# Kernel optimization log

Hardware: AMD Instinct MI355X
Metric: run time of the kernel (lower is better)

Reference implementation:

```python
import jax, jax.numpy as jnp
import numpy as np

H = 12            # num_heads
GRID = 14         # sqrt(num_patches)
NP_ = GRID * GRID # num_patches = 196


def _relative_position_index():
    coords = np.stack(np.meshgrid(np.arange(GRID), np.arange(GRID), indexing='ij'))  # [2,14,14]
    flat = coords.reshape(2, -1)                                   # [2,196]
    rel = flat[:, :, None] - flat[:, None, :]                      # [2,196,196]
    rel = rel.transpose(1, 2, 0).astype(np.int32)                  # [196,196,2]
    rel[..., 0] += GRID - 1
    rel[..., 1] += GRID - 1
    rel[..., 0] *= 2 * GRID - 1
    return rel.sum(-1)                                             # [196,196] in [0,729)


def setup_inputs() -> dict:
    key = jax.random.key(0)
    k1, k2, k3, k4 = jax.random.split(key, 4)
    B, N, C = 64, NP_ + 1, 768
    return {
        'x': jax.random.normal(k1, (B, N, C), dtype=jnp.float32),
        'w_qkv': jax.random.normal(k2, (3 * C, C), dtype=jnp.float32) * 0.02,
        'w_proj': jax.random.normal(k3, (C, C), dtype=jnp.float32) * 0.02,
        'b_proj': jnp.zeros((C,), dtype=jnp.float32),
        # torch inits the table to zeros; use small randn so the bias path is exercised
        'rpb_table': jax.random.normal(k4, ((2 * GRID - 1) ** 2, H), dtype=jnp.float32) * 0.02,
        'rel_idx': jnp.asarray(_relative_position_index()),
    }


def reference(x, w_qkv, w_proj, b_proj, rpb_table, rel_idx):
    B, N, C = x.shape
    hd = C // H
    scale = hd ** -0.5
    qkv = (x @ w_qkv.T).reshape(B, N, 3, H, hd).transpose(2, 0, 3, 1, 4)  # [3,B,H,N,hd]
    q, k, v = qkv[0] * scale, qkv[1], qkv[2]
    attn = jnp.einsum('bhqd,bhkd->bhqk', q, k)                            # [B,H,N,N]
    bias = rpb_table[rel_idx.reshape(-1)].reshape(NP_, NP_, H).transpose(2, 0, 1)  # [H,196,196]
    attn = attn.at[:, :, 1:, 1:].add(bias[None])                          # skip CLS row/col
    attn = jax.nn.softmax(attn, axis=-1)
    out = jnp.einsum('bhqk,bhkd->bqhd', attn, v).reshape(B, N, C)
    return out @ w_proj.T + b_proj
```

## Files before the change

### kernel.cpp

```cpp
#include <hip/hip_runtime.h>

typedef float f32x4 __attribute__((ext_vector_type(4)));
typedef short short8 __attribute__((ext_vector_type(8)));

#define DEVI static __device__ __forceinline__

DEVI ushort f2bf(float f) {
  unsigned u = __builtin_bit_cast(unsigned, f);
  u += 0x7fffu + ((u >> 16) & 1u);
  return (ushort)(u >> 16);
}

DEVI short8 pack8(float4 a, float4 b) {
  union { ushort u[8]; short8 v; } t;
  t.u[0] = f2bf(a.x); t.u[1] = f2bf(a.y); t.u[2] = f2bf(a.z); t.u[3] = f2bf(a.w);
  t.u[4] = f2bf(b.x); t.u[5] = f2bf(b.y); t.u[6] = f2bf(b.z); t.u[7] = f2bf(b.w);
  return t.v;
}

DEVI f32x4 MFMA16(short8 a, short8 b, f32x4 c) {
  return __builtin_amdgcn_mfma_f32_16x16x32_bf16(a, b, c, 0, 0, 0);
}

DEVI void gld16(const ushort* g, ushort* l) {
  __builtin_amdgcn_global_load_lds(
      (const __attribute__((address_space(1))) unsigned int*)g,
      (__attribute__((address_space(3))) unsigned int*)l, 16, 0, 0);
}

__global__ void prep_all(const float* __restrict__ table, const int* __restrict__ rel_idx,
                         float* __restrict__ bias,
                         const float* __restrict__ x, ushort* __restrict__ xbf,
                         const float* __restrict__ wq, ushort* __restrict__ wqb,
                         const float* __restrict__ wp, ushort* __restrict__ wpb) {
  const int bid = blockIdx.x, tid = threadIdx.x;
  if (bid < 2028) {
    int i = bid * 256 + tid;
    int k = i % 208;
    int t = i / 208;
    int q = t % 208;
    int h = t / 208;
    float v;
    if (k >= 197) v = -1e30f;
    else if (q == 0 || k == 0 || q >= 197) v = 0.0f;
    else v = table[rel_idx[(q - 1) * 196 + (k - 1)] * 12 + h];
    bias[i] = v;
  } else if (bid < 6756) {
    int i = (bid - 2028) * 256 + tid;
    float4 a = ((const float4*)x)[i * 2];
    float4 b = ((const float4*)x)[i * 2 + 1];
    ((short8*)xbf)[i] = pack8(a, b);
  } else if (bid < 7620) {
    int i = (bid - 6756) * 256 + tid;
    float4 a = ((const float4*)wq)[i * 2];
    float4 b = ((const float4*)wq)[i * 2 + 1];
    ((short8*)wqb)[i] = pack8(a, b);
  } else {
    int i = (bid - 7620) * 256 + tid;
    float4 a = ((const float4*)wp)[i * 2];
    float4 b = ((const float4*)wp)[i * 2 + 1];
    ((short8*)wpb)[i] = pack8(a, b);
  }
}

#define BARRIER() { asm volatile("" ::: "memory"); __builtin_amdgcn_s_barrier(); asm volatile("" ::: "memory"); }
#define VMC(N) asm volatile("s_waitcnt vmcnt(" #N ")" ::: "memory")
#define NOP

template <int MODE, int NBN>
__launch_bounds__(512, 2)
__global__ void gemm8p(const ushort* __restrict__ A, const ushort* __restrict__ B,
                       ushort* __restrict__ q, ushort* __restrict__ k,
                       ushort* __restrict__ v,
                       const float* __restrict__ bprj, float* __restrict__ out) {
  __shared__ __align__(16) ushort AS[32768];
  __shared__ __align__(16) ushort BS[32768];

  const int tid = threadIdx.x;
  const int lane = tid & 63, wid = tid >> 6;
  const int wm = wid >> 2, wn = wid & 3;
  const int l15 = lane & 15, l4 = lane >> 4;

  const int nwg = gridDim.x;
  const int qc = nwg >> 3, rc = nwg & 7;
  const int xcd = blockIdx.x & 7, sub = blockIdx.x >> 3;
  const int wgid = (xcd < rc ? xcd * (qc + 1) : rc * (qc + 1) + (xcd - rc) * qc) + sub;
  const int bn = wgid % NBN, bm = wgid / NBN;

  const int lr = lane >> 3;
  const int cg = lane & 7;
  const ushort* pa[2][2];
  const ushort* pb[2][2];
#pragma unroll
  for (int h = 0; h < 2; h++) {
#pragma unroll
    for (int j = 0; j < 2; j++) {
      int rhl = wid * 8 + lr + j * 64;
      int scol = (cg ^ (rhl & 7)) * 8;
      long garow = (long)bm * 256 + (rhl >> 4) * 32 + h * 16 + (rhl & 15);
      if (garow > 12607) garow = 12607;
      pa[h][j] = A + garow * 768 + scol;
      pb[h][j] = B + ((long)bn * 256 + h * 128 + rhl) * 768 + scol;
    }
  }

  const int cs0 = (l4 * 8) ^ ((l15 & 7) << 3);

  f32x4 acc[8][4];
#pragma unroll
  for (int m = 0; m < 8; m++)
#pragma unroll
    for (int n = 0; n < 4; n++) acc[m][n] = (f32x4)0.0f;

#define SA(BUF, H, KT) { gld16(pa[H][0] + (KT) * 64, AS + (BUF) * 16384 + (H) * 8192 + wid * 512);        \
                         gld16(pa[H][1] + (KT) * 64, AS + (BUF) * 16384 + (H) * 8192 + wid * 512 + 4096); }
#define SB(BUF, H, KT) { gld16(pb[H][0] + (KT) * 64, BS + (BUF) * 16384 + (H) * 8192 + wid * 512);        \
                         gld16(pb[H][1] + (KT) * 64, BS + (BUF) * 16384 + (H) * 8192 + wid * 512 + 4096); }

#define PHASE(BUF, FH, KK, STG, WAITC)                                                        \
  {                                                                                           \
    short8 af[4], bv[4];                                                                      \
    const int cko = cs0 ^ ((KK) << 5);                                                        \
    _Pragma("unroll") for (int j = 0; j < 4; j++)                                             \
      af[j] = *(const short8*)&AS[(BUF) * 16384 + (FH) * 8192 + (wm * 4 + j) * 1024 +         \
                                  l15 * 64 + cko];                                            \
    _Pragma("unroll") for (int n = 0; n < 4; n++)                                             \
      bv[n] = *(const short8*)&BS[(BUF) * 16384 + (wn >> 1) * 8192 +                          \
                                  ((wn & 1) * 64 + n * 16 + l15) * 64 + cko];                 \
    STG;                                                                                      \
    WAITC;                                                                                    \
    BARRIER();                                                                                \
    __builtin_amdgcn_s_setprio(1);                                                            \
    _Pragma("unroll") for (int j = 0; j < 4; j++)                                             \
      _Pragma("unroll") for (int n = 0; n < 4; n++)                                           \
        acc[(FH) + 2 * j][n] = MFMA16(af[j], bv[n], acc[(FH) + 2 * j][n]);                    \
    __builtin_amdgcn_s_setprio(0);                                                            \
    BARRIER();                                                                                \
  }

  SA(0, 0, 0) SA(0, 1, 0) SB(0, 0, 0) SB(0, 1, 0) SA(1, 0, 1)
  VMC(2);
  BARRIER();

  for (int i = 0; i < 5; ++i) {
    const int t1 = 2 * i + 1, t2 = 2 * i + 2, t3 = 2 * i + 3;
    PHASE(0, 0, 0, SA(1, 1, t1), NOP)
    PHASE(0, 1, 0, SB(1, 0, t1), NOP)
    PHASE(0, 0, 1, SB(1, 1, t1), NOP)
    PHASE(0, 1, 1, SA(0, 0, t2), VMC(2))
    PHASE(1, 0, 0, SA(0, 1, t2), NOP)
    PHASE(1, 1, 0, SB(0, 0, t2), NOP)
    PHASE(1, 0, 1, SB(0, 1, t2), NOP)
    PHASE(1, 1, 1, SA(1, 0, t3), VMC(2))
  }
  PHASE(0, 0, 0, SA(1, 1, 11), NOP)
  PHASE(0, 1, 0, SB(1, 0, 11), NOP)
  PHASE(0, 0, 1, SB(1, 1, 11), NOP)
  PHASE(0, 1, 1, NOP, VMC(0))
  PHASE(1, 0, 0, NOP, NOP)
  PHASE(1, 1, 0, NOP, NOP)
  PHASE(1, 0, 1, NOP, NOP)
  PHASE(1, 1, 1, NOP, NOP)

  if (MODE == 0) {
    const int c6 = (bn * 256 + wn * 64) >> 6;
    const int s = c6 / 12, hh = c6 % 12;
    ushort* dst = (s == 0) ? q : ((s == 1) ? k : v);
    const float qs = (s == 0) ? 0.125f : 1.0f;
#pragma unroll
    for (int f = 0; f < 8; f++) {
#pragma unroll
      for (int r = 0; r < 4; r++) {
        int gm = bm * 256 + wm * 128 + f * 16 + l4 * 4 + r;
        if (gm >= 12608) continue;
        int b = gm / 197;
        int ns = gm - b * 197;
        size_t base = (size_t)((b * 12 + hh) * 197 + ns) * 64;
#pragma unroll
        for (int n = 0; n < 4; n++)
          dst[base + n * 16 + l15] = f2bf(acc[f][n][r] * qs);
      }
    }
  } else {
    float bb[4];
#pragma unroll
    for (int n = 0; n < 4; n++) bb[n] = bprj[bn * 256 + wn * 64 + n * 16 + l15];
#pragma unroll
    for (int f = 0; f < 8; f++) {
#pragma unroll
      for (int r = 0; r < 4; r++) {
        int gm = bm * 256 + wm * 128 + f * 16 + l4 * 4 + r;
        if (gm >= 12608) continue;
#pragma unroll
        for (int n = 0; n < 4; n++)
          out[(size_t)gm * 768 + bn * 256 + wn * 64 + n * 16 + l15] = acc[f][n][r] + bb[n];
      }
    }
  }
#undef SA
#undef SB
#undef PHASE
}

__launch_bounds__(512)
__global__ void attn(const ushort* __restrict__ qws, const ushort* __restrict__ kws,
                     const ushort* __restrict__ vws, const float* __restrict__ biasws,
                     ushort* __restrict__ aout) {
  __shared__ __align__(16) ushort Ks[208 * 72];
  __shared__ __align__(16) ushort Vt[64 * 232];
  __shared__ __align__(16) ushort Ps[8 * 16 * 232];

  const int bh = blockIdx.x;
  const int b = bh / 12;
  const int h = bh - b * 12;
  const ushort* qb = qws + (size_t)bh * 197 * 64;
  const ushort* kb = kws + (size_t)bh * 197 * 64;
  const ushort* vb = vws + (size_t)bh * 197 * 64;

  const int tid = threadIdx.x;
  const int lane = tid & 63, wid = tid >> 6;
  const int l15 = lane & 15, l4 = lane >> 4;

  for (int c = tid; c < 208 * 8; c += 512) {
    int n = c >> 3, col = (c & 7) << 3;
    short8 v = (short8)0;
    if (n < 197) v = *(const short8*)(kb + n * 64 + col);
    *(short8*)&Ks[n * 72 + col] = v;
  }
  for (int c = tid; c < 224 * 8; c += 512) {
    int n = c % 224;
    int d0 = (c / 224) << 3;
    ushort tmp[8] = {0, 0, 0, 0, 0, 0, 0, 0};
    if (n < 197) {
      short8 v = *(const short8*)(vb + n * 64 + d0);
#pragma unroll
      for (int j = 0; j < 8; j++) tmp[j] = (ushort)v[j];
    }
#pragma unroll
    for (int j = 0; j < 8; j++) Vt[(d0 + j) * 232 + n] = tmp[j];
  }
  __syncthreads();

  ushort* pb = &Ps[wid * (16 * 232)];
  const float* biasb = biasws + (size_t)h * 208 * 208;

  for (int t = wid; t < 13; t += 8) {
    const int q0 = t * 16;
    int qr = q0 + l15; if (qr > 196) qr = 196;
    short8 aq0 = *(const short8*)(qb + qr * 64 + (l4 << 3));
    short8 aq1 = *(const short8*)(qb + qr * 64 + 32 + (l4 << 3));

    f32x4 sc[13];
    __builtin_amdgcn_s_setprio(1);
#pragma unroll
    for (int ct = 0; ct < 13; ct++) {
      short8 b0 = *(const short8*)&Ks[(ct * 16 + l15) * 72 + (l4 << 3)];
      short8 b1 = *(const short8*)&Ks[(ct * 16 + l15) * 72 + 32 + (l4 << 3)];
      f32x4 s = (f32x4)0.0f;
      s = MFMA16(aq0, b0, s);
      s = MFMA16(aq1, b1, s);
      sc[ct] = s;
    }
    __builtin_amdgcn_s_setprio(0);

    float mx[4] = {-1e38f, -1e38f, -1e38f, -1e38f};
#pragma unroll
    for (int ct = 0; ct < 13; ct++) {
#pragma unroll
      for (int r = 0; r < 4; r++) {
        float bv = biasb[(q0 + l4 * 4 + r) * 208 + ct * 16 + l15];
        float v = sc[ct][r] + bv;
        sc[ct][r] = v;
        mx[r] = fmaxf(mx[r], v);
      }
    }
#pragma unroll
    for (int r = 0; r < 4; r++) {
      mx[r] = fmaxf(mx[r], __shfl_xor(mx[r], 1));
      mx[r] = fmaxf(mx[r], __shfl_xor(mx[r], 2));
      mx[r] = fmaxf(mx[r], __shfl_xor(mx[r], 4));
      mx[r] = fmaxf(mx[r], __shfl_xor(mx[r], 8));
    }
    float sum[4] = {0.f, 0.f, 0.f, 0.f};
#pragma unroll
    for (int ct = 0; ct < 13; ct++) {
#pragma unroll
      for (int r = 0; r < 4; r++) {
        float p = __expf(sc[ct][r] - mx[r]);
        sc[ct][r] = p;
        sum[r] += p;
      }
    }
#pragma unroll
    for (int r = 0; r < 4; r++) {
      sum[r] += __shfl_xor(sum[r], 1);
      sum[r] += __shfl_xor(sum[r], 2);
      sum[r] += __shfl_xor(sum[r], 4);
      sum[r] += __shfl_xor(sum[r], 8);
    }

#pragma unroll
    for (int ct = 0; ct < 13; ct++)
#pragma unroll
      for (int r = 0; r < 4; r++)
        pb[(l4 * 4 + r) * 232 + ct * 16 + l15] = f2bf(sc[ct][r]);
#pragma unroll
    for (int r = 0; r < 4; r++)
      pb[(l4 * 4 + r) * 232 + 208 + l15] = 0;

    short8 pa[7];
#pragma unroll
    for (int kk = 0; kk < 7; kk++)
      pa[kk] = *(const short8*)&pb[l15 * 232 + kk * 32 + (l4 << 3)];
    f32x4 o[4];
    __builtin_amdgcn_s_setprio(1);
#pragma unroll
    for (int dt = 0; dt < 4; dt++) {
      f32x4 acc = (f32x4)0.0f;
#pragma unroll
      for (int kk = 0; kk < 7; kk++) {
        short8 bv = *(const short8*)&Vt[(dt * 16 + l15) * 232 + kk * 32 + (l4 << 3)];
        acc = MFMA16(pa[kk], bv, acc);
      }
      o[dt] = acc;
    }
    __builtin_amdgcn_s_setprio(0);

    float rs[4];
#pragma unroll
    for (int r = 0; r < 4; r++) rs[r] = 1.0f / sum[r];
#pragma unroll
    for (int dt = 0; dt < 4; dt++) {
#pragma unroll
      for (int r = 0; r < 4; r++) {
        int row = q0 + l4 * 4 + r;
        if (row < 197) {
          float v = o[dt][r] * rs[r];
          aout[(size_t)(b * 197 + row) * 768 + h * 64 + dt * 16 + l15] = f2bf(v);
        }
      }
    }
  }
}

extern "C" void kernel_launch(void* const* d_in, const int* in_sizes, int n_in,
                              void* d_out, int out_size, void* d_ws, size_t ws_size,
                              hipStream_t stream) {
  const float* x      = (const float*)d_in[0];
  const float* w_qkv  = (const float*)d_in[1];
  const float* w_proj = (const float*)d_in[2];
  const float* b_proj = (const float*)d_in[3];
  const float* rpb    = (const float*)d_in[4];
  const int*   relidx = (const int*)d_in[5];
  float* out = (float*)d_out;

  char* ws = (char*)d_ws;
  const size_t HB = (size_t)12608 * 768 * 2;
  ushort* xbf   = (ushort*)(ws);
  ushort* qws   = (ushort*)(ws + HB);
  ushort* kws   = (ushort*)(ws + 2 * HB);
  ushort* vws   = (ushort*)(ws + 3 * HB);
  float*  bias  = (float*)(ws + 4 * HB);
  ushort* wqkvb = (ushort*)(ws + 4 * HB + 2076672);
  ushort* wprjb = (ushort*)(ws + 4 * HB + 2076672 + 3538944);
  ushort* aout  = xbf;

  hipLaunchKernelGGL(prep_all, dim3(7908), dim3(256), 0, stream,
                     rpb, relidx, bias, x, xbf, w_qkv, wqkvb, w_proj, wprjb);
  hipLaunchKernelGGL((gemm8p<0, 9>), dim3(9 * 50), dim3(512), 0, stream,
                     xbf, wqkvb, qws, kws, vws, nullptr, nullptr);
  hipLaunchKernelGGL(attn, dim3(768), dim3(512), 0, stream, qws, kws, vws, bias, aout);
  hipLaunchKernelGGL((gemm8p<1, 3>), dim3(3 * 50), dim3(512), 0, stream,
                     aout, wprjb, nullptr, nullptr, nullptr, b_proj, out);
}
```

Before: 147.7 us.

## Restructure GEMM LDS tiling into quadrant phases and store bias as bf16

Reworks the GEMM main loop so each phase computes a 64x32 quadrant over the full 64-wide k-slice. Staging loads are regrouped per quadrant with a new swizzle, and vmcnt waits are tuned so loads overlap with MFMAs more finely. Separately, the relative-position bias buffer is stored as bf16 instead of fp32, halving its reads in the attention kernel. The bf16 bias loses some precision, and the -1e30 mask value is rounded to bf16.

Result: no change. 149.6 us (+1.3%).

```diff
diff --git a/kernel.cpp b/kernel.cpp
--- a/kernel.cpp
+++ b/kernel.cpp
@@ -9,6 +9,11 @@
   unsigned u = __builtin_bit_cast(unsigned, f);
   u += 0x7fffu + ((u >> 16) & 1u);
   return (ushort)(u >> 16);
+}
+
+DEVI float b2f(ushort u) {
+  unsigned x = ((unsigned)u) << 16;
+  return __builtin_bit_cast(float, x);
 }
 
 DEVI short8 pack8(float4 a, float4 b) {
@@ -28,8 +33,11 @@
       (__attribute__((address_space(3))) unsigned int*)l, 16, 0, 0);
 }
 
+#define VMC(N) asm volatile("s_waitcnt vmcnt(" #N ")" ::: "memory")
+#define LGK0() asm volatile("s_waitcnt lgkmcnt(0)" ::: "memory")
+
 __global__ void prep_all(const float* __restrict__ table, const int* __restrict__ rel_idx,
-                         float* __restrict__ bias,
+                         ushort* __restrict__ bias,
                          const float* __restrict__ x, ushort* __restrict__ xbf,
                          const float* __restrict__ wq, ushort* __restrict__ wqb,
                          const float* __restrict__ wp, ushort* __restrict__ wpb) {
@@ -44,7 +52,7 @@
     if (k >= 197) v = -1e30f;
     else if (q == 0 || k == 0 || q >= 197) v = 0.0f;
     else v = table[rel_idx[(q - 1) * 196 + (k - 1)] * 12 + h];
-    bias[i] = v;
+    bias[i] = f2bf(v);
   } else if (bid < 6756) {
     int i = (bid - 2028) * 256 + tid;
     float4 a = ((const float4*)x)[i * 2];
@@ -63,16 +71,12 @@
   }
 }
 
-#define BARRIER() { asm volatile("" ::: "memory"); __builtin_amdgcn_s_barrier(); asm volatile("" ::: "memory"); }
-#define VMC(N) asm volatile("s_waitcnt vmcnt(" #N ")" ::: "memory")
-#define NOP
-
 template <int MODE, int NBN>
 __launch_bounds__(512, 2)
-__global__ void gemm8p(const ushort* __restrict__ A, const ushort* __restrict__ B,
-                       ushort* __restrict__ q, ushort* __restrict__ k,
-                       ushort* __restrict__ v,
-                       const float* __restrict__ bprj, float* __restrict__ out) {
+__global__ void gemm8(const ushort* __restrict__ A, const ushort* __restrict__ B,
+                      ushort* __restrict__ q, ushort* __restrict__ k,
+                      ushort* __restrict__ v,
+                      const float* __restrict__ bprj, float* __restrict__ out) {
   __shared__ __align__(16) ushort AS[32768];
   __shared__ __align__(16) ushort BS[32768];
 
@@ -87,24 +91,28 @@
   const int wgid = (xcd < rc ? xcd * (qc + 1) : rc * (qc + 1) + (xcd - rc) * qc) + sub;
   const int bn = wgid % NBN, bm = wgid / NBN;
 
-  const int lr = lane >> 3;
-  const int cg = lane & 7;
+  const int sr = lane >> 3;
+  const int scol = ((lane & 7) ^ sr) << 3;
   const ushort* pa[2][2];
-  const ushort* pb[2][2];
+  const ushort* pbv[2][2];
+  int la[2][2], lb[2][2];
 #pragma unroll
   for (int h = 0; h < 2; h++) {
 #pragma unroll
     for (int j = 0; j < 2; j++) {
-      int rhl = wid * 8 + lr + j * 64;
-      int scol = (cg ^ (rhl & 7)) * 8;
-      long garow = (long)bm * 256 + (rhl >> 4) * 32 + h * 16 + (rhl & 15);
-      if (garow > 12607) garow = 12607;
-      pa[h][j] = A + garow * 768 + scol;
-      pb[h][j] = B + ((long)bn * 256 + h * 128 + rhl) * 768 + scol;
-    }
-  }
-
-  const int cs0 = (l4 * 8) ^ ((l15 & 7) << 3);
+      int rowA = j * 128 + h * 64 + wid * 8 + sr;
+      long ga = (long)bm * 256 + rowA;
+      if (ga > 12607) ga = 12607;
+      pa[h][j] = A + ga * 768 + scol;
+      la[h][j] = h * 4096 + wid * 512 + j * 8192;
+      int rowB = j * 128 + (wid >> 2) * 64 + h * 32 + (wid & 3) * 8 + sr;
+      pbv[h][j] = B + ((long)bn * 256 + rowB) * 768 + scol;
+      lb[h][j] = (wid >> 2) * 4096 + h * 2048 + (wid & 3) * 512 + j * 8192;
+    }
+  }
+
+  const int c0 = ((l4 ^ (l15 & 7)) << 3);
+  const int c1 = (((4 | l4) ^ (l15 & 7)) << 3);
 
   f32x4 acc[8][4];
 #pragma unroll
@@ -112,55 +120,66 @@
 #pragma unroll
     for (int n = 0; n < 4; n++) acc[m][n] = (f32x4)0.0f;
 
-#define SA(BUF, H, KT) { gld16(pa[H][0] + (KT) * 64, AS + (BUF) * 16384 + (H) * 8192 + wid * 512);        \
-                         gld16(pa[H][1] + (KT) * 64, AS + (BUF) * 16384 + (H) * 8192 + wid * 512 + 4096); }
-#define SB(BUF, H, KT) { gld16(pb[H][0] + (KT) * 64, BS + (BUF) * 16384 + (H) * 8192 + wid * 512);        \
-                         gld16(pb[H][1] + (KT) * 64, BS + (BUF) * 16384 + (H) * 8192 + wid * 512 + 4096); }
-
-#define PHASE(BUF, FH, KK, STG, WAITC)                                                        \
-  {                                                                                           \
-    short8 af[4], bv[4];                                                                      \
-    const int cko = cs0 ^ ((KK) << 5);                                                        \
-    _Pragma("unroll") for (int j = 0; j < 4; j++)                                             \
-      af[j] = *(const short8*)&AS[(BUF) * 16384 + (FH) * 8192 + (wm * 4 + j) * 1024 +         \
-                                  l15 * 64 + cko];                                            \
-    _Pragma("unroll") for (int n = 0; n < 4; n++)                                             \
-      bv[n] = *(const short8*)&BS[(BUF) * 16384 + (wn >> 1) * 8192 +                          \
-                                  ((wn & 1) * 64 + n * 16 + l15) * 64 + cko];                 \
-    STG;                                                                                      \
-    WAITC;                                                                                    \
-    BARRIER();                                                                                \
-    __builtin_amdgcn_s_setprio(1);                                                            \
-    _Pragma("unroll") for (int j = 0; j < 4; j++)                                             \
-      _Pragma("unroll") for (int n = 0; n < 4; n++)                                           \
-        acc[(FH) + 2 * j][n] = MFMA16(af[j], bv[n], acc[(FH) + 2 * j][n]);                    \
-    __builtin_amdgcn_s_setprio(0);                                                            \
-    BARRIER();                                                                                \
-  }
-
-  SA(0, 0, 0) SA(0, 1, 0) SB(0, 0, 0) SB(0, 1, 0) SA(1, 0, 1)
-  VMC(2);
-  BARRIER();
+#define STA(BUF, H, KO) { gld16(pa[H][0] + (KO), AS + (BUF) * 16384 + la[H][0]); \
+                          gld16(pa[H][1] + (KO), AS + (BUF) * 16384 + la[H][1]); }
+#define STB(BUF, H, KO) { gld16(pbv[H][0] + (KO), BS + (BUF) * 16384 + lb[H][0]); \
+                          gld16(pbv[H][1] + (KO), BS + (BUF) * 16384 + lb[H][1]); }
+
+#define PHASE(BUF, MQ, NQ, STG, WAITC)                                          \
+  {                                                                             \
+    __builtin_amdgcn_sched_barrier(0);                                          \
+    short8 af0[4], af1[4], bq0[2], bq1[2];                                      \
+    const int abo = (BUF) * 16384 + (wm * 128 + (MQ) * 64 + l15) * 64;          \
+    const int bbo = (BUF) * 16384 + (wn * 64 + (NQ) * 32 + l15) * 64;           \
+    _Pragma("unroll") for (int j = 0; j < 4; j++)                               \
+      af0[j] = *(const short8*)&AS[abo + j * 1024 + c0];                        \
+    _Pragma("unroll") for (int j = 0; j < 4; j++)                               \
+      af1[j] = *(const short8*)&AS[abo + j * 1024 + c1];                        \
+    _Pragma("unroll") for (int n = 0; n < 2; n++)                               \
+      bq0[n] = *(const short8*)&BS[bbo + n * 1024 + c0];                        \
+    _Pragma("unroll") for (int n = 0; n < 2; n++)                               \
+      bq1[n] = *(const short8*)&BS[bbo + n * 1024 + c1];                        \
+    STG                                                                         \
+    WAITC;                                                                      \
+    __builtin_amdgcn_s_barrier();                                               \
+    LGK0();                                                                     \
+    __builtin_amdgcn_sched_barrier(0);                                          \
+    __builtin_amdgcn_s_setprio(1);                                              \
+    _Pragma("unroll") for (int j = 0; j < 4; j++)                               \
+      _Pragma("unroll") for (int n = 0; n < 2; n++) {                           \
+        acc[(MQ) * 4 + j][(NQ) * 2 + n] =                                       \
+            MFMA16(af0[j], bq0[n], acc[(MQ) * 4 + j][(NQ) * 2 + n]);            \
+        acc[(MQ) * 4 + j][(NQ) * 2 + n] =                                       \
+            MFMA16(af1[j], bq1[n], acc[(MQ) * 4 + j][(NQ) * 2 + n]);            \
+      }                                                                         \
+    __builtin_amdgcn_s_setprio(0);                                              \
+    __builtin_amdgcn_s_barrier();                                               \
+  }
+
+  STA(0, 0, 0) STB(0, 0, 0) STA(0, 1, 0) STB(0, 1, 0)
+  STA(1, 0, 64) STB(1, 0, 64)
+  VMC(8);
+  __builtin_amdgcn_s_barrier();
 
   for (int i = 0; i < 5; ++i) {
-    const int t1 = 2 * i + 1, t2 = 2 * i + 2, t3 = 2 * i + 3;
-    PHASE(0, 0, 0, SA(1, 1, t1), NOP)
-    PHASE(0, 1, 0, SB(1, 0, t1), NOP)
-    PHASE(0, 0, 1, SB(1, 1, t1), NOP)
-    PHASE(0, 1, 1, SA(0, 0, t2), VMC(2))
-    PHASE(1, 0, 0, SA(0, 1, t2), NOP)
-    PHASE(1, 1, 0, SB(0, 0, t2), NOP)
-    PHASE(1, 0, 1, SB(0, 1, t2), NOP)
-    PHASE(1, 1, 1, SA(1, 0, t3), VMC(2))
-  }
-  PHASE(0, 0, 0, SA(1, 1, 11), NOP)
-  PHASE(0, 1, 0, SB(1, 0, 11), NOP)
-  PHASE(0, 0, 1, SB(1, 1, 11), NOP)
-  PHASE(0, 1, 1, NOP, VMC(0))
-  PHASE(1, 0, 0, NOP, NOP)
-  PHASE(1, 1, 0, NOP, NOP)
-  PHASE(1, 0, 1, NOP, NOP)
-  PHASE(1, 1, 1, NOP, NOP)
+    const int t1 = (2 * i + 1) * 64, t2 = (2 * i + 2) * 64, t3 = (2 * i + 3) * 64;
+    PHASE(0, 0, 0, STA(1, 1, t1), VMC(6))
+    PHASE(0, 0, 1, STB(1, 1, t1), VMC(10))
+    PHASE(0, 1, 0, STA(0, 0, t2), ((void)0))
+    PHASE(0, 1, 1, STB(0, 0, t2), VMC(8))
+    PHASE(1, 0, 0, STA(0, 1, t2), VMC(6))
+    PHASE(1, 0, 1, STB(0, 1, t2), VMC(10))
+    PHASE(1, 1, 0, STA(1, 0, t3), ((void)0))
+    PHASE(1, 1, 1, STB(1, 0, t3), VMC(8))
+  }
+  PHASE(0, 0, 0, STA(1, 1, 704), VMC(6))
+  PHASE(0, 0, 1, STB(1, 1, 704), VMC(10))
+  PHASE(0, 1, 0, ((void)0);, ((void)0))
+  PHASE(0, 1, 1, ((void)0);, VMC(4))
+  PHASE(1, 0, 0, ((void)0);, VMC(0))
+  PHASE(1, 0, 1, ((void)0);, ((void)0))
+  PHASE(1, 1, 0, ((void)0);, ((void)0))
+  PHASE(1, 1, 1, ((void)0);, ((void)0))
 
   if (MODE == 0) {
     const int c6 = (bn * 256 + wn * 64) >> 6;
@@ -197,14 +216,14 @@
       }
     }
   }
-#undef SA
-#undef SB
+#undef STA
+#undef STB
 #undef PHASE
 }
 
 __launch_bounds__(512)
 __global__ void attn(const ushort* __restrict__ qws, const ushort* __restrict__ kws,
-                     const ushort* __restrict__ vws, const float* __restrict__ biasws,
+                     const ushort* __restrict__ vws, const ushort* __restrict__ biasws,
                      ushort* __restrict__ aout) {
   __shared__ __align__(16) ushort Ks[208 * 72];
   __shared__ __align__(16) ushort Vt[64 * 232];
@@ -242,7 +261,7 @@
   __syncthreads();
 
   ushort* pb = &Ps[wid * (16 * 232)];
-  const float* biasb = biasws + (size_t)h * 208 * 208;
+  const ushort* biasb = biasws + (size_t)h * 208 * 208;
 
   for (int t = wid; t < 13; t += 8) {
     const int q0 = t * 16;
@@ -268,7 +287,7 @@
     for (int ct = 0; ct < 13; ct++) {
 #pragma unroll
       for (int r = 0; r < 4; r++) {
-        float bv = biasb[(q0 + l4 * 4 + r) * 208 + ct * 16 + l15];
+        float bv = b2f(biasb[(q0 + l4 * 4 + r) * 208 + ct * 16 + l15]);
         float v = sc[ct][r] + bv;
         sc[ct][r] = v;
         mx[r] = fmaxf(mx[r], v);
@@ -360,16 +379,16 @@
   ushort* qws   = (ushort*)(ws + HB);
   ushort* kws   = (ushort*)(ws + 2 * HB);
   ushort* vws   = (ushort*)(ws + 3 * HB);
-  float*  bias  = (float*)(ws + 4 * HB);
+  ushort* bias  = (ushort*)(ws + 4 * HB);
   ushort* wqkvb = (ushort*)(ws + 4 * HB + 2076672);
   ushort* wprjb = (ushort*)(ws + 4 * HB + 2076672 + 3538944);
   ushort* aout  = xbf;
 
   hipLaunchKernelGGL(prep_all, dim3(7908), dim3(256), 0, stream,
                      rpb, relidx, bias, x, xbf, w_qkv, wqkvb, w_proj, wprjb);
-  hipLaunchKernelGGL((gemm8p<0, 9>), dim3(9 * 50), dim3(512), 0, stream,
+  hipLaunchKernelGGL((gemm8<0, 9>), dim3(50 * 9), dim3(512), 0, stream,
                      xbf, wqkvb, qws, kws, vws, nullptr, nullptr);
   hipLaunchKernelGGL(attn, dim3(768), dim3(512), 0, stream, qws, kws, vws, bias, aout);
-  hipLaunchKernelGGL((gemm8p<1, 3>), dim3(3 * 50), dim3(512), 0, stream,
+  hipLaunchKernelGGL((gemm8<1, 3>), dim3(50 * 3), dim3(512), 0, stream,
                      aout, wprjb, nullptr, nullptr, nullptr, b_proj, out);
 }
```
